# Kernel tuning notes

Hardware: AMD Instinct MI355X
Metric: run time of the kernel (lower is better)

## Reference

```python
import jax, jax.numpy as jnp
import numpy as np

N, G = 10000, 200          # nodes, graphs
EL, EG = 160000, 500000    # local / global edges
S, V = 256, 64             # scalar / vector hidden dims
NA, NB = 16, 5             # atom types, bond types


def _lin(k, i, o):
    return (jax.random.normal(k, (i, o), jnp.float32) / np.sqrt(i))


def scatter_mean(vals, idx, num_segments):
    # vals: [N, ...]; idx: [N] int
    sums = jax.ops.segment_sum(vals, idx, num_segments=num_segments)
    cnt = jax.ops.segment_sum(jnp.ones((vals.shape[0],), vals.dtype), idx,
                              num_segments=num_segments)
    cnt = jnp.maximum(cnt, 1.0).reshape((-1,) + (1,) * (vals.ndim - 1))
    return sums / cnt


def calc_edge_attrs(edge_index, pos):
    src, tgt = edge_index[0], edge_index[1]
    r = pos[tgt] - pos[src]                      # [E,3]
    a = (pos[tgt] * pos[src]).sum(-1)            # [E]
    d = jnp.sqrt(jnp.clip((r ** 2).sum(-1), 1e-6))
    r_norm = r / d[:, None]
    return d, a, r_norm


def setup_inputs() -> dict:
    key = jax.random.key(0)
    ks = jax.random.split(key, 24)
    inp = {}
    inp["x"] = jax.random.normal(ks[0], (N, NA), jnp.float32)
    inp["t"] = jax.random.uniform(ks[1], (G, 1), jnp.float32)
    inp["pos"] = jax.random.normal(ks[2], (N, 3), jnp.float32)
    eil = jax.random.randint(ks[3], (2, EL), 0, N)
    eig = jax.random.randint(ks[4], (2, EG), 0, N)
    # avoid self-edges so edge distances are strictly positive (safe sqrt grads)
    eig = eig.at[1].set(jnp.where(eig[1] == eig[0], (eig[1] + 1) % N, eig[1]))
    eil = eil.at[1].set(jnp.where(eil[1] == eil[0], (eil[1] + 1) % N, eil[1]))
    inp["edge_index_local"] = eil
    inp["edge_index_global"] = eig
    inp["edge_attr_global"] = jax.random.normal(ks[5], (EG, NB), jnp.float32)
    inp["batch"] = jnp.sort(jax.random.randint(ks[6], (N,), 0, G))
    # learned parameters
    inp["W_time"], inp["b_time"] = _lin(ks[7], 1, S), jnp.zeros((S,), jnp.float32)
    inp["W_atom"], inp["b_atom"] = _lin(ks[8], NA, S), jnp.zeros((S,), jnp.float32)
    inp["W_at"], inp["b_at"] = _lin(ks[9], S, S), jnp.zeros((S,), jnp.float32)
    inp["W_shared"], inp["b_shared"] = _lin(ks[10], S, S), jnp.zeros((S,), jnp.float32)
    inp["W_b0"], inp["b_b0"] = _lin(ks[11], S + 1, S), jnp.zeros((S,), jnp.float32)
    inp["W_b1"], inp["b_b1"] = _lin(ks[12], S, 2 * NB), jnp.zeros((2 * NB,), jnp.float32)
    inp["W_coord"] = _lin(ks[13], V, 2)           # no bias
    inp["W_atoms"], inp["b_atoms"] = _lin(ks[14], S, 2 * NA), jnp.zeros((2 * NA,), jnp.float32)
    return inp


def reference(x, t, pos, edge_attr_global, W_time, b_time, W_atom, b_atom,
              W_at, b_at, W_shared, b_shared, W_b0, b_b0, W_b1, b_b1,
              W_coord, W_atoms, b_atoms,
              edge_index_local, edge_index_global, batch):
    # --- trunk: center positions, embed atoms + time ---
    pos = pos - scatter_mean(pos, batch, G)[batch]
    temb = t @ W_time + b_time                    # [G,S]
    tnode = temb[batch]                           # [N,S]
    s = x @ W_atom + b_atom
    s = (s + tnode) @ W_at + b_at                 # [N,S]
    # --- edge attrs (gather-compute pattern feeding the GNN) ---
    d_l, a_l, rn_l = calc_edge_attrs(edge_index_local, pos)
    d_g, a_g, rn_g = calc_edge_attrs(edge_index_global, pos)
    # GNN stand-in (identity on s, v, p): v initialized to zeros as in original
    v = jnp.zeros((N, 3, V), s.dtype)
    # --- prediction head ---
    s = jax.nn.silu(s @ W_shared + b_shared)
    j, i = edge_index_global[0], edge_index_global[1]
    d = jnp.sqrt(((pos[i] - pos[j]) ** 2).sum(-1, keepdims=True))  # [EG,1]
    edge = jnp.concatenate([s[i] + s[j], d], axis=-1)              # [EG,S+1]
    bonds = jax.nn.silu(edge @ W_b0 + b_b0) @ W_b1 + b_b1          # [EG,2*NB]
    bonds_pred, bonds_eps = bonds[:, :NB], bonds[:, NB:]
    coords = jnp.einsum('nkv,vo->nko', v, W_coord)                 # [N,3,2]
    coords = coords - scatter_mean(coords, batch, G)[batch]
    coords_eps0, coords_eps1 = coords[..., 0], coords[..., 1]      # [N,3]
    atoms = s @ W_atoms + b_atoms                                  # [N,2*NA]
    atoms_eps, atoms_pred = atoms[:, :NA], atoms[:, NA:]
    pos_c = pos - scatter_mean(pos, batch, G)[batch]
    coords_pred = pos_c + coords_eps1
    return (coords_pred, coords_eps0, atoms_pred, atoms_eps,
            bonds_pred, bonds_eps, d_l, rn_l, a_g, rn_g)
```

## Files before the change

kernel.cpp:

```cpp
#include <hip/hip_runtime.h>
#include <hip/hip_bf16.h>

typedef __hip_bfloat16 bf16;
typedef short bf16x8 __attribute__((ext_vector_type(8)));
typedef float f32x4 __attribute__((ext_vector_type(4)));
typedef float f32x2 __attribute__((ext_vector_type(2)));

#define N_NODES  10000
#define G_GRAPHS 200
#define EL_EDGES 160000
#define EG_EDGES 500000
#define S_DIM    256
#define APAD     264

#define BONDS_BLOCKS 15625
#define LOCAL_BLOCKS 625
#define B1ROW    280

#define WS_FLAG   0
#define WS_POSC   1024
#define WS_WD     31232
#define WS_BB1    34304
#define WS_WATOM  34560
#define WS_WTIME  38656
#define WS_BTIME  38912
#define WS_BATOM  39168
#define WS_BAT    39424
#define WS_BSH    39680
#define WS_BATOMS 39936
#define WS_T      40000
#define WS_X      40448
#define WT_AT     200448
#define WT_SH     233216
#define WT_B0     265984
#define WT_ATOMS  298752
#define WS_B1F8   302848
#define WS_H      303968
#define WS_BB0R   943968
#define WS_END_FLOATS 944224

#define CHAN(S)    ((((S) >> 6) << 6) + (((S) & 3) << 4) + (((S) & 63) >> 2))
#define CHANINV(k) ((((k) >> 6) << 6) + (((k) & 15) << 2) + (((k) >> 4) & 3))

#define O_CPRED 0
#define O_CEPS  30000
#define O_APRED 60000
#define O_AEPS  220000
#define O_BPRED 380000
#define O_BEPS  2880000
#define O_DL    5380000
#define O_RNL   5540000
#define O_AG    6020000
#define O_RNG   6520000

__device__ __forceinline__ float b2f(bf16 v) { return __bfloat162float(v); }
__device__ __forceinline__ bf16  f2b(float v) { return __float2bfloat16(v); }
__device__ __forceinline__ unsigned short bbits(float v) {
    bf16 b = f2b(v);
    return *reinterpret_cast<unsigned short*>(&b);
}
__device__ __forceinline__ float ldin(const void* p, int idx, int isf32) {
    return isf32 ? ((const float*)p)[idx] : b2f(((const bf16*)p)[idx]);
}
__device__ __forceinline__ void stout(void* out, int f32o, size_t idx, float v) {
    if (f32o) ((float*)out)[idx] = v;
    else      ((bf16*)out)[idx]  = f2b(v);
}
__device__ __forceinline__ float silu(float p) {
    return p * __builtin_amdgcn_rcpf(1.0f + __expf(-p));
}
__device__ __forceinline__ int dtype_f32(const void* tt) {
    const unsigned short* q = (const unsigned short*)tt;
    int c = 0;
#pragma unroll
    for (int z = 0; z < 32; ++z) c += (q[z] >= 0x4000) ? 1 : 0;
    return c > 0;
}

__global__ void k_prep(const void* __restrict__ x, const void* __restrict__ tt,
                       const void* __restrict__ W_time, const void* __restrict__ b_time,
                       const void* __restrict__ W_atom, const void* __restrict__ b_atom,
                       const void* __restrict__ W_at, const void* __restrict__ b_at,
                       const void* __restrict__ W_shared, const void* __restrict__ b_shared,
                       const void* __restrict__ W_b0, const void* __restrict__ b_b0,
                       const void* __restrict__ W_b1, const void* __restrict__ b_b1,
                       const void* __restrict__ W_atoms, const void* __restrict__ b_atoms,
                       float* __restrict__ ws) {
    const int t = blockIdx.x * blockDim.x + threadIdx.x;
    const int f = dtype_f32(tt);
    if (t == 0) ws[WS_FLAG] = f ? 1.0f : 0.0f;
    if (t < 65536) {
        const int k = t >> 8, n = t & 255;
        ((unsigned short*)(ws + WT_AT))[n * 256 + k] = bbits(ldin(W_at, t, f));
        ((unsigned short*)(ws + WT_SH))[n * 256 + k] = bbits(ldin(W_shared, t, f));
        ((unsigned short*)(ws + WT_B0))[n * 256 + k] = bbits(ldin(W_b0, t, f));
    }
    if (t < 160000) ws[WS_X + t] = ldin(x, t, f);
    if (t < 8192) {
        const int k = t >> 5, n = t & 31;
        ((unsigned short*)(ws + WT_ATOMS))[n * 256 + k] = bbits(ldin(W_atoms, t, f));
    }
    if (t < 4480) {
        const int n = t / B1ROW, s = t - n * B1ROW;
        float v = (n < 10 && s < 256) ? ldin(W_b1, CHAN(s) * 10 + n, f) : 0.0f;
        int enc = __builtin_amdgcn_cvt_pk_fp8_f32(v, 0.0f, 0, false);
        ((unsigned char*)(ws + WS_B1F8))[t] = (unsigned char)(enc & 0xff);
    }
    if (t < 4096) ws[WS_WATOM + t] = ldin(W_atom, t, f);
    if (t < 256) {
        ws[WS_WD + t]   = ldin(W_b0, 65536 + CHAN(t), f);
        ws[WS_BB0R + t] = ldin(b_b0, t, f);
        ws[WS_WTIME + t] = ldin(W_time, t, f);
        ws[WS_BTIME + t] = ldin(b_time, t, f);
        ws[WS_BATOM + t] = ldin(b_atom, t, f);
        ws[WS_BAT + t]   = ldin(b_at, t, f);
        ws[WS_BSH + t]   = ldin(b_shared, t, f);
    }
    if (t < 200) ws[WS_T + t] = ldin(tt, t, f);
    if (t < 32)  ws[WS_BATOMS + t] = ldin(b_atoms, t, f);
    if (t < 16)  ws[WS_BB1 + t] = (t < 10) ? ldin(b_b1, t, f) : 0.0f;
}

__global__ void k_pos(const void* __restrict__ pos, const int* __restrict__ batch,
                      float* __restrict__ ws, void* __restrict__ out) {
    const int g = blockIdx.x;
    const int f32o = ws[WS_FLAG] != 0.0f;
    __shared__ int s_lo, s_hi;
    __shared__ float wsum[4][3];
    __shared__ float mean[3];
    if (threadIdx.x == 0) {
        int lo = 0, hi = N_NODES;
        while (lo < hi) { int m = (lo + hi) >> 1; if (batch[m] < g) lo = m + 1; else hi = m; }
        s_lo = lo;
        int lo2 = lo; hi = N_NODES;
        while (lo2 < hi) { int m = (lo2 + hi) >> 1; if (batch[m] < g + 1) lo2 = m + 1; else hi = m; }
        s_hi = lo2;
    }
    __syncthreads();
    const int lo = s_lo, hi = s_hi, cnt = hi - lo;
    float sx = 0.f, sy = 0.f, sz = 0.f;
    for (int n = lo + threadIdx.x; n < hi; n += 256) {
        sx += ldin(pos, n * 3 + 0, f32o);
        sy += ldin(pos, n * 3 + 1, f32o);
        sz += ldin(pos, n * 3 + 2, f32o);
    }
#pragma unroll
    for (int off = 32; off > 0; off >>= 1) {
        sx += __shfl_down(sx, off);
        sy += __shfl_down(sy, off);
        sz += __shfl_down(sz, off);
    }
    if ((threadIdx.x & 63) == 0) {
        wsum[threadIdx.x >> 6][0] = sx;
        wsum[threadIdx.x >> 6][1] = sy;
        wsum[threadIdx.x >> 6][2] = sz;
    }
    __syncthreads();
    if (threadIdx.x == 0) {
        float inv = 1.0f / (float)max(cnt, 1);
        mean[0] = (wsum[0][0] + wsum[1][0] + wsum[2][0] + wsum[3][0]) * inv;
        mean[1] = (wsum[0][1] + wsum[1][1] + wsum[2][1] + wsum[3][1]) * inv;
        mean[2] = (wsum[0][2] + wsum[1][2] + wsum[2][2] + wsum[3][2]) * inv;
    }
    __syncthreads();
    for (int n = lo + threadIdx.x; n < hi; n += 256) {
#pragma unroll
        for (int k = 0; k < 3; ++k) {
            float p = ldin(pos, n * 3 + k, f32o) - mean[k];
            ws[WS_POSC + n * 3 + k] = p;
            stout(out, f32o, O_CPRED + n * 3 + k, p);
            stout(out, f32o, O_CEPS + n * 3 + k, 0.0f);
        }
    }
}

__global__ __launch_bounds__(256) void k_node(
    const int* __restrict__ batch, const float* __restrict__ ws,
    unsigned int* __restrict__ h_out, void* __restrict__ out) {
    __shared__ unsigned short actA[16][APAD];
    __shared__ unsigned short actB[16][APAD];
    const int tid = threadIdx.x;
    const int wave = tid >> 6, lane = tid & 63;
    const int quad = lane >> 4, l16 = lane & 15;
    const int row0 = blockIdx.x * 16;

    {
        const int r = tid >> 4;
        const int c0 = (tid & 15) * 16;
        const int g = row0 + r;
        float tb = ws[WS_T + batch[g]];
        float xr[16];
#pragma unroll
        for (int k = 0; k < 16; ++k) xr[k] = ws[WS_X + g * 16 + k];
        for (int cc = 0; cc < 16; cc += 4) {
            const int c = c0 + cc;
            float a0 = ws[WS_BATOM + c + 0] + tb * ws[WS_WTIME + c + 0] + ws[WS_BTIME + c + 0];
            float a1 = ws[WS_BATOM + c + 1] + tb * ws[WS_WTIME + c + 1] + ws[WS_BTIME + c + 1];
            float a2 = ws[WS_BATOM + c + 2] + tb * ws[WS_WTIME + c + 2] + ws[WS_BTIME + c + 2];
            float a3 = ws[WS_BATOM + c + 3] + tb * ws[WS_WTIME + c + 3] + ws[WS_BTIME + c + 3];
#pragma unroll
            for (int k = 0; k < 16; ++k) {
                float4 w4 = *(const float4*)(ws + WS_WATOM + k * S_DIM + c);
                a0 += xr[k] * w4.x; a1 += xr[k] * w4.y;
                a2 += xr[k] * w4.z; a3 += xr[k] * w4.w;
            }
            actA[r][c + 0] = bbits(a0); actA[r][c + 1] = bbits(a1);
            actA[r][c + 2] = bbits(a2); actA[r][c + 3] = bbits(a3);
        }
    }
    __syncthreads();

    const unsigned short* wt_at = (const unsigned short*)(ws + WT_AT);
    const unsigned short* wt_sh = (const unsigned short*)(ws + WT_SH);
    const unsigned short* wt_b0 = (const unsigned short*)(ws + WT_B0);
    const unsigned short* wt_am = (const unsigned short*)(ws + WT_ATOMS);
    const int n0 = wave * 64;

    {
        f32x4 acc[4] = {};
        for (int kk = 0; kk < S_DIM; kk += 32) {
            const int k = kk + quad * 8;
            bf16x8 a = *(const bf16x8*)&actA[l16][k];
#pragma unroll
            for (int nt = 0; nt < 4; ++nt) {
                bf16x8 b = *(const bf16x8*)(wt_at + (size_t)(n0 + nt * 16 + l16) * S_DIM + k);
                acc[nt] = __builtin_amdgcn_mfma_f32_16x16x32_bf16(a, b, acc[nt], 0, 0, 0);
            }
        }
#pragma unroll
        for (int nt = 0; nt < 4; ++nt) {
            const int n = n0 + nt * 16 + l16;
            const float bv = ws[WS_BAT + n];
#pragma unroll
            for (int r = 0; r < 4; ++r)
                actB[quad * 4 + r][n] = bbits(acc[nt][r] + bv);
        }
    }
    __syncthreads();

    {
        f32x4 acc[4] = {};
        for (int kk = 0; kk < S_DIM; kk += 32) {
            const int k = kk + quad * 8;
            bf16x8 a = *(const bf16x8*)&actB[l16][k];
#pragma unroll
            for (int nt = 0; nt < 4; ++nt) {
                bf16x8 b = *(const bf16x8*)(wt_sh + (size_t)(n0 + nt * 16 + l16) * S_DIM + k);
                acc[nt] = __builtin_amdgcn_mfma_f32_16x16x32_bf16(a, b, acc[nt], 0, 0, 0);
            }
        }
        __syncthreads();
#pragma unroll
        for (int nt = 0; nt < 4; ++nt) {
            const int n = n0 + nt * 16 + l16;
            const float bv = ws[WS_BSH + n];
#pragma unroll
            for (int r = 0; r < 4; ++r)
                actA[quad * 4 + r][n] = bbits(silu(acc[nt][r] + bv));
        }
    }
    __syncthreads();

    {
        f32x4 acc[4] = {};
        for (int kk = 0; kk < S_DIM; kk += 32) {
            const int k = kk + quad * 8;
            bf16x8 a = *(const bf16x8*)&actA[l16][k];
#pragma unroll
            for (int nt = 0; nt < 4; ++nt) {
                bf16x8 b = *(const bf16x8*)(wt_b0 + (size_t)(n0 + nt * 16 + l16) * S_DIM + k);
                acc[nt] = __builtin_amdgcn_mfma_f32_16x16x32_bf16(a, b, acc[nt], 0, 0, 0);
            }
        }
        float bh[4];
#pragma unroll
        for (int nt = 0; nt < 4; ++nt) bh[nt] = 0.5f * ws[WS_BB0R + n0 + nt * 16 + l16];
#pragma unroll
        for (int r = 0; r < 4; ++r) {
            const int g = row0 + quad * 4 + r;
            int w = 0;
            w = __builtin_amdgcn_cvt_pk_fp8_f32(acc[0][r] + bh[0], acc[1][r] + bh[1], w, false);
            w = __builtin_amdgcn_cvt_pk_fp8_f32(acc[2][r] + bh[2], acc[3][r] + bh[3], w, true);
            h_out[(size_t)g * 64 + wave * 16 + l16] = (unsigned int)w;
        }
    }

    if (wave < 2) {
        f32x4 acc = {};
        const int n = wave * 16 + l16;
        for (int kk = 0; kk < S_DIM; kk += 32) {
            const int k = kk + quad * 8;
            bf16x8 a = *(const bf16x8*)&actA[l16][k];
            bf16x8 b = *(const bf16x8*)(wt_am + (size_t)n * S_DIM + k);
            acc = __builtin_amdgcn_mfma_f32_16x16x32_bf16(a, b, acc, 0, 0, 0);
        }
        const float bv = ws[WS_BATOMS + n];
        const int f32o = ws[WS_FLAG] != 0.0f;
#pragma unroll
        for (int r = 0; r < 4; ++r) {
            const int g = row0 + quad * 4 + r;
            float v = acc[r] + bv;
            if (n < 16) stout(out, f32o, O_AEPS + (size_t)g * 16 + n, v);
            else        stout(out, f32o, O_APRED + (size_t)g * 16 + (n - 16), v);
        }
    }
}

__global__ __launch_bounds__(256, 7) void k_edges(const int* __restrict__ eig,
                                                  const int* __restrict__ eil,
                                                  const float* __restrict__ ws,
                                                  const unsigned char* __restrict__ h,
                                                  void* __restrict__ out) {
    __shared__ unsigned char sm[2][32][272];
    __shared__ float cwd[256];
    __shared__ long cwb1l[16 * B1ROW / 8];
    unsigned char* cwb1 = (unsigned char*)cwb1l;
    const int f32o = ws[WS_FLAG] != 0.0f;

    if (blockIdx.x >= BONDS_BLOCKS) {
        const int e = (blockIdx.x - BONDS_BLOCKS) * 256 + threadIdx.x;
        const float* posc = ws + WS_POSC;
        const int s = eil[e];
        const int t = eil[EL_EDGES + e];
        float rx = posc[t * 3 + 0] - posc[s * 3 + 0];
        float ry = posc[t * 3 + 1] - posc[s * 3 + 1];
        float rz = posc[t * 3 + 2] - posc[s * 3 + 2];
        float dsq = rx * rx + ry * ry + rz * rz;
        float d = sqrtf(fmaxf(dsq, 1e-6f));
        float inv = 1.0f / d;
        stout(out, f32o, O_DL + e, d);
        stout(out, f32o, O_RNL + (size_t)e * 3 + 0, rx * inv);
        stout(out, f32o, O_RNL + (size_t)e * 3 + 1, ry * inv);
        stout(out, f32o, O_RNL + (size_t)e * 3 + 2, rz * inv);
        return;
    }

    {
        const int t = threadIdx.x;
        cwd[t] = ws[WS_WD + t];
        const unsigned int* src = (const unsigned int*)(ws + WS_B1F8);
        unsigned int* dst = (unsigned int*)cwb1;
        for (int q = t; q < 16 * B1ROW / 4; q += 256) dst[q] = src[q];
    }

    const int wave = threadIdx.x >> 6, lane = threadIdx.x & 63;
    const int quad = lane >> 4, l16 = lane & 15;
    const int P = wave >> 1, sub = wave & 1;
    const int e0 = blockIdx.x * 32 + P * 16;

    uint4 tmp[4];
#pragma unroll
    for (int p = 0; p < 4; ++p) {
        const int r16 = p * 4 + quad;
        const int es = e0 + r16;
        const int node = sub ? eig[es] : eig[EG_EDGES + es];
        tmp[p] = *(const uint4*)(h + (size_t)node * 256 + l16 * 16);
    }
#pragma unroll
    for (int p = 0; p < 4; ++p) {
        const int row = sub * 16 + p * 4 + quad;
        *(uint4*)&sm[P][row][l16 * 16] = tmp[p];
    }

    if (sub == 0) {
        const int e = e0 + l16;
        const int j = eig[e];
        const int i = eig[EG_EDGES + e];
        const float* posc = ws + WS_POSC;
        float pix = posc[i * 3 + 0], piy = posc[i * 3 + 1], piz = posc[i * 3 + 2];
        float pjx = posc[j * 3 + 0], pjy = posc[j * 3 + 1], pjz = posc[j * 3 + 2];
        float rx = pix - pjx, ry = piy - pjy, rz = piz - pjz;
        float dsq = rx * rx + ry * ry + rz * rz;
        if (quad == 0) {
            float ag = pix * pjx + piy * pjy + piz * pjz;
            float inv = 1.0f / sqrtf(fmaxf(dsq, 1e-6f));
            stout(out, f32o, O_AG + e, ag);
            stout(out, f32o, O_RNG + (size_t)e * 3 + 0, rx * inv);
            stout(out, f32o, O_RNG + (size_t)e * 3 + 1, ry * inv);
            stout(out, f32o, O_RNG + (size_t)e * 3 + 2, rz * inv);
            *(float*)&sm[P][l16][256] = sqrtf(dsq);
        }
    }
    __syncthreads();

    const float d = *(const float*)&sm[P][l16][256];
    const unsigned char* cw = cwb1 + (size_t)l16 * B1ROW;

    const int kbase = sub * 128;
    f32x4 acc = {};
#pragma unroll
    for (int t = 0; t < 4; ++t) {
        const int k = kbase + t * 32 + quad * 8;
        uint2 uaw = *(const uint2*)&sm[P][l16][k];
        uint2 ubw = *(const uint2*)&sm[P][16 + l16][k];
        float4 wA = *(const float4*)(cwd + k);
        float4 wB = *(const float4*)(cwd + k + 4);
        f32x2 a01 = __builtin_amdgcn_cvt_pk_f32_fp8((int)uaw.x, false);
        f32x2 a23 = __builtin_amdgcn_cvt_pk_f32_fp8((int)uaw.x, true);
        f32x2 a45 = __builtin_amdgcn_cvt_pk_f32_fp8((int)uaw.y, false);
        f32x2 a67 = __builtin_amdgcn_cvt_pk_f32_fp8((int)uaw.y, true);
        f32x2 b01 = __builtin_amdgcn_cvt_pk_f32_fp8((int)ubw.x, false);
        f32x2 b23 = __builtin_amdgcn_cvt_pk_f32_fp8((int)ubw.x, true);
        f32x2 b45 = __builtin_amdgcn_cvt_pk_f32_fp8((int)ubw.y, false);
        f32x2 b67 = __builtin_amdgcn_cvt_pk_f32_fp8((int)ubw.y, true);
        float u0 = silu(fmaf(d, wA.x, a01.x + b01.x));
        float u1 = silu(fmaf(d, wA.y, a01.y + b01.y));
        float u2 = silu(fmaf(d, wA.z, a23.x + b23.x));
        float u3 = silu(fmaf(d, wA.w, a23.y + b23.y));
        float u4 = silu(fmaf(d, wB.x, a45.x + b45.x));
        float u5 = silu(fmaf(d, wB.y, a45.y + b45.y));
        float u6 = silu(fmaf(d, wB.z, a67.x + b67.x));
        float u7 = silu(fmaf(d, wB.w, a67.y + b67.y));
        int lo = __builtin_amdgcn_cvt_pk_fp8_f32(u0, u1, 0, false);
        lo = __builtin_amdgcn_cvt_pk_fp8_f32(u2, u3, lo, true);
        int hi = __builtin_amdgcn_cvt_pk_fp8_f32(u4, u5, 0, false);
        hi = __builtin_amdgcn_cvt_pk_fp8_f32(u6, u7, hi, true);
        long a64 = (long)(((unsigned long)(unsigned int)hi << 32) | (unsigned int)lo);
        long b64 = *(const long*)(cw + k);
        acc = __builtin_amdgcn_mfma_f32_16x16x32_fp8_fp8(a64, b64, acc, 0, 0, 0);
    }

    __syncthreads();
    f32x4* sc = (f32x4*)&sm[P][0][0];
    if (sub == 1) sc[lane] = acc;
    __syncthreads();
    if (sub == 0 && l16 < 10) {
        f32x4 o = sc[lane];
        const float bv = ws[WS_BB1 + l16];
#pragma unroll
        for (int r = 0; r < 4; ++r) {
            const int er = e0 + quad * 4 + r;
            float v = acc[r] + o[r] + bv;
            if (l16 < 5) stout(out, f32o, O_BPRED + (size_t)er * 5 + l16, v);
            else         stout(out, f32o, O_BEPS + (size_t)er * 5 + (l16 - 5), v);
        }
    }
}

extern "C" void kernel_launch(void* const* d_in, const int* in_sizes, int n_in,
                              void* d_out, int out_size, void* d_ws, size_t ws_size,
                              hipStream_t stream) {
    const void* x        = d_in[0];
    const void* t        = d_in[1];
    const void* pos      = d_in[2];
    const int*  eil      = (const int*)d_in[3];
    const int*  eig      = (const int*)d_in[4];
    const int*  batch    = (const int*)d_in[6];
    const void* W_time   = d_in[7];
    const void* b_time   = d_in[8];
    const void* W_atom   = d_in[9];
    const void* b_atom   = d_in[10];
    const void* W_at     = d_in[11];
    const void* b_at     = d_in[12];
    const void* W_shared = d_in[13];
    const void* b_shared = d_in[14];
    const void* W_b0     = d_in[15];
    const void* b_b0     = d_in[16];
    const void* W_b1     = d_in[17];
    const void* b_b1     = d_in[18];
    const void* W_atoms  = d_in[20];
    const void* b_atoms  = d_in[21];
    (void)in_sizes; (void)n_in; (void)out_size;

    const size_t NEED = (size_t)WS_END_FLOATS * sizeof(float);
    if (ws_size < NEED) return;

    float* ws = (float*)d_ws;
    unsigned int* hbuf = (unsigned int*)(ws + WS_H);

    k_prep<<<640, 256, 0, stream>>>(x, t, W_time, b_time, W_atom, b_atom,
                                    W_at, b_at, W_shared, b_shared, W_b0, b_b0,
                                    W_b1, b_b1, W_atoms, b_atoms, ws);
    k_pos<<<G_GRAPHS, 256, 0, stream>>>(pos, batch, ws, d_out);
    k_node<<<N_NODES / 16, 256, 0, stream>>>(batch, ws, hbuf, d_out);
    k_edges<<<BONDS_BLOCKS + LOCAL_BLOCKS, 256, 0, stream>>>(
        eig, eil, ws, (const unsigned char*)hbuf, d_out);
}
```

Before: 224.4 us.

## Switch edge bond MLP to fp16 gathers with packed half silu and f16 MFMA

The per-node hidden projection is now stored as fp16 instead of fp8, and the edge kernel gathers both endpoint rows directly from global memory. One wave now handles 16 edges over the full K=256, so the LDS staging, the two-wave split-K and its reduction barriers are gone. The silu is computed in packed half precision with v_exp_f16/v_rcp_f16, and the second layer uses f16 MFMA with a pre-swizzled fp16 W_b1. This removes fp8 conversions and block syncs, but doubles gather bytes per edge and lowers the occupancy hint from 7 to 4.

```diff
diff --git a/kernel.cpp b/kernel.cpp
--- a/kernel.cpp
+++ b/kernel.cpp
@@ -4,7 +4,8 @@
 typedef __hip_bfloat16 bf16;
 typedef short bf16x8 __attribute__((ext_vector_type(8)));
 typedef float f32x4 __attribute__((ext_vector_type(4)));
-typedef float f32x2 __attribute__((ext_vector_type(2)));
+typedef _Float16 f16x2 __attribute__((ext_vector_type(2)));
+typedef _Float16 f16x8 __attribute__((ext_vector_type(8)));
 
 #define N_NODES  10000
 #define G_GRAPHS 200
@@ -13,13 +14,14 @@
 #define S_DIM    256
 #define APAD     264
 
-#define BONDS_BLOCKS 15625
-#define LOCAL_BLOCKS 625
-#define B1ROW    280
+#define BONDS2        7813
+#define LOCAL_BLOCKS  625
 
 #define WS_FLAG   0
 #define WS_POSC   1024
-#define WS_WD     31232
+#define WS_WDH    31232
+#define WS_W1F    31488
+#define WS_BB0R   33536
 #define WS_BB1    34304
 #define WS_WATOM  34560
 #define WS_WTIME  38656
@@ -34,13 +36,8 @@
 #define WT_SH     233216
 #define WT_B0     265984
 #define WT_ATOMS  298752
-#define WS_B1F8   302848
 #define WS_H      303968
-#define WS_BB0R   943968
-#define WS_END_FLOATS 944224
-
-#define CHAN(S)    ((((S) >> 6) << 6) + (((S) & 3) << 4) + (((S) & 63) >> 2))
-#define CHANINV(k) ((((k) >> 6) << 6) + (((k) & 15) << 2) + (((k) >> 4) & 3))
+#define WS_END_FLOATS 1583968
 
 #define O_CPRED 0
 #define O_CEPS  30000
@@ -59,6 +56,10 @@
     bf16 b = f2b(v);
     return *reinterpret_cast<unsigned short*>(&b);
 }
+__device__ __forceinline__ unsigned short h16bits(float v) {
+    _Float16 h = (_Float16)v;
+    return *reinterpret_cast<unsigned short*>(&h);
+}
 __device__ __forceinline__ float ldin(const void* p, int idx, int isf32) {
     return isf32 ? ((const float*)p)[idx] : b2f(((const bf16*)p)[idx]);
 }
@@ -68,6 +69,21 @@
 }
 __device__ __forceinline__ float silu(float p) {
     return p * __builtin_amdgcn_rcpf(1.0f + __expf(-p));
+}
+__device__ __forceinline__ _Float16 h_exp2(_Float16 x) {
+    _Float16 r;
+    asm("v_exp_f16 %0, %1" : "=v"(r) : "v"(x));
+    return r;
+}
+__device__ __forceinline__ _Float16 h_rcp(_Float16 x) {
+    _Float16 r;
+    asm("v_rcp_f16 %0, %1" : "=v"(r) : "v"(x));
+    return r;
+}
+__device__ __forceinline__ _Float16 h_silu(_Float16 p) {
+    const _Float16 nlog2e = (_Float16)(-1.44269504f);
+    _Float16 ex = h_exp2(p * nlog2e);
+    return p * h_rcp((_Float16)1.0f + ex);
 }
 __device__ __forceinline__ int dtype_f32(const void* tt) {
     const unsigned short* q = (const unsigned short*)tt;
@@ -100,15 +116,15 @@
         const int k = t >> 5, n = t & 31;
         ((unsigned short*)(ws + WT_ATOMS))[n * 256 + k] = bbits(ldin(W_atoms, t, f));
     }
-    if (t < 4480) {
-        const int n = t / B1ROW, s = t - n * B1ROW;
-        float v = (n < 10 && s < 256) ? ldin(W_b1, CHAN(s) * 10 + n, f) : 0.0f;
-        int enc = __builtin_amdgcn_cvt_pk_fp8_f32(v, 0.0f, 0, false);
-        ((unsigned char*)(ws + WS_B1F8))[t] = (unsigned char)(enc & 0xff);
+    if (t < 4096) {
+        const int i = t & 7, l16 = (t >> 3) & 15, quad = (t >> 7) & 3, ts = t >> 9;
+        const int k = ts * 32 + quad * 8 + i;
+        float v = (l16 < 10) ? ldin(W_b1, k * 10 + l16, f) : 0.0f;
+        ((unsigned short*)(ws + WS_W1F))[t] = h16bits(v);
     }
     if (t < 4096) ws[WS_WATOM + t] = ldin(W_atom, t, f);
     if (t < 256) {
-        ws[WS_WD + t]   = ldin(W_b0, 65536 + CHAN(t), f);
+        ((unsigned short*)(ws + WS_WDH))[t] = h16bits(ldin(W_b0, 65536 + t, f));
         ws[WS_BB0R + t] = ldin(b_b0, t, f);
         ws[WS_WTIME + t] = ldin(W_time, t, f);
         ws[WS_BTIME + t] = ldin(b_time, t, f);
@@ -176,7 +192,7 @@
 
 __global__ __launch_bounds__(256) void k_node(
     const int* __restrict__ batch, const float* __restrict__ ws,
-    unsigned int* __restrict__ h_out, void* __restrict__ out) {
+    unsigned short* __restrict__ h_out, void* __restrict__ out) {
     __shared__ unsigned short actA[16][APAD];
     __shared__ unsigned short actB[16][APAD];
     const int tid = threadIdx.x;
@@ -272,16 +288,16 @@
                 acc[nt] = __builtin_amdgcn_mfma_f32_16x16x32_bf16(a, b, acc[nt], 0, 0, 0);
             }
         }
-        float bh[4];
-#pragma unroll
-        for (int nt = 0; nt < 4; ++nt) bh[nt] = 0.5f * ws[WS_BB0R + n0 + nt * 16 + l16];
-#pragma unroll
-        for (int r = 0; r < 4; ++r) {
-            const int g = row0 + quad * 4 + r;
-            int w = 0;
-            w = __builtin_amdgcn_cvt_pk_fp8_f32(acc[0][r] + bh[0], acc[1][r] + bh[1], w, false);
-            w = __builtin_amdgcn_cvt_pk_fp8_f32(acc[2][r] + bh[2], acc[3][r] + bh[3], w, true);
-            h_out[(size_t)g * 64 + wave * 16 + l16] = (unsigned int)w;
+        _Float16* hp = (_Float16*)h_out;
+#pragma unroll
+        for (int nt = 0; nt < 4; ++nt) {
+            const int n = n0 + nt * 16 + l16;
+            const float bh = 0.5f * ws[WS_BB0R + n];
+#pragma unroll
+            for (int r = 0; r < 4; ++r) {
+                const int g = row0 + quad * 4 + r;
+                hp[(size_t)g * 256 + n] = (_Float16)(acc[nt][r] + bh);
+            }
         }
     }
 
@@ -306,19 +322,17 @@
     }
 }
 
-__global__ __launch_bounds__(256, 7) void k_edges(const int* __restrict__ eig,
+union H8 { f16x8 v; f16x2 p[4]; };
+
+__global__ __launch_bounds__(256, 4) void k_edges(const int* __restrict__ eig,
                                                   const int* __restrict__ eil,
                                                   const float* __restrict__ ws,
-                                                  const unsigned char* __restrict__ h,
+                                                  const _Float16* __restrict__ h,
                                                   void* __restrict__ out) {
-    __shared__ unsigned char sm[2][32][272];
-    __shared__ float cwd[256];
-    __shared__ long cwb1l[16 * B1ROW / 8];
-    unsigned char* cwb1 = (unsigned char*)cwb1l;
     const int f32o = ws[WS_FLAG] != 0.0f;
 
-    if (blockIdx.x >= BONDS_BLOCKS) {
-        const int e = (blockIdx.x - BONDS_BLOCKS) * 256 + threadIdx.x;
+    if (blockIdx.x >= BONDS2) {
+        const int e = (blockIdx.x - BONDS2) * 256 + threadIdx.x;
         const float* posc = ws + WS_POSC;
         const int s = eil[e];
         const int t = eil[EL_EDGES + e];
@@ -335,102 +349,63 @@
         return;
     }
 
-    {
-        const int t = threadIdx.x;
-        cwd[t] = ws[WS_WD + t];
-        const unsigned int* src = (const unsigned int*)(ws + WS_B1F8);
-        unsigned int* dst = (unsigned int*)cwb1;
-        for (int q = t; q < 16 * B1ROW / 4; q += 256) dst[q] = src[q];
-    }
-
     const int wave = threadIdx.x >> 6, lane = threadIdx.x & 63;
     const int quad = lane >> 4, l16 = lane & 15;
-    const int P = wave >> 1, sub = wave & 1;
-    const int e0 = blockIdx.x * 32 + P * 16;
-
-    uint4 tmp[4];
-#pragma unroll
-    for (int p = 0; p < 4; ++p) {
-        const int r16 = p * 4 + quad;
-        const int es = e0 + r16;
-        const int node = sub ? eig[es] : eig[EG_EDGES + es];
-        tmp[p] = *(const uint4*)(h + (size_t)node * 256 + l16 * 16);
-    }
-#pragma unroll
-    for (int p = 0; p < 4; ++p) {
-        const int row = sub * 16 + p * 4 + quad;
-        *(uint4*)&sm[P][row][l16 * 16] = tmp[p];
-    }
-
-    if (sub == 0) {
-        const int e = e0 + l16;
-        const int j = eig[e];
-        const int i = eig[EG_EDGES + e];
-        const float* posc = ws + WS_POSC;
-        float pix = posc[i * 3 + 0], piy = posc[i * 3 + 1], piz = posc[i * 3 + 2];
-        float pjx = posc[j * 3 + 0], pjy = posc[j * 3 + 1], pjz = posc[j * 3 + 2];
-        float rx = pix - pjx, ry = piy - pjy, rz = piz - pjz;
-        float dsq = rx * rx + ry * ry + rz * rz;
-        if (quad == 0) {
-            float ag = pix * pjx + piy * pjy + piz * pjz;
-            float inv = 1.0f / sqrtf(fmaxf(dsq, 1e-6f));
-            stout(out, f32o, O_AG + e, ag);
-            stout(out, f32o, O_RNG + (size_t)e * 3 + 0, rx * inv);
-            stout(out, f32o, O_RNG + (size_t)e * 3 + 1, ry * inv);
-            stout(out, f32o, O_RNG + (size_t)e * 3 + 2, rz * inv);
-            *(float*)&sm[P][l16][256] = sqrtf(dsq);
-        }
-    }
-    __syncthreads();
-
-    const float d = *(const float*)&sm[P][l16][256];
-    const unsigned char* cw = cwb1 + (size_t)l16 * B1ROW;
-
-    const int kbase = sub * 128;
+    const int e0 = blockIdx.x * 64 + wave * 16;
+    if (e0 >= EG_EDGES) return;
+
+    const int e = e0 + l16;
+    const int j = eig[e];
+    const int i = eig[EG_EDGES + e];
+
+    const float* posc = ws + WS_POSC;
+    float pix = posc[i * 3 + 0], piy = posc[i * 3 + 1], piz = posc[i * 3 + 2];
+    float pjx = posc[j * 3 + 0], pjy = posc[j * 3 + 1], pjz = posc[j * 3 + 2];
+    float rx = pix - pjx, ry = piy - pjy, rz = piz - pjz;
+    float dsq = rx * rx + ry * ry + rz * rz;
+    float dbf = sqrtf(dsq);
+    if (quad == 0) {
+        float ag = pix * pjx + piy * pjy + piz * pjz;
+        float inv = 1.0f / sqrtf(fmaxf(dsq, 1e-6f));
+        stout(out, f32o, O_AG + e, ag);
+        stout(out, f32o, O_RNG + (size_t)e * 3 + 0, rx * inv);
+        stout(out, f32o, O_RNG + (size_t)e * 3 + 1, ry * inv);
+        stout(out, f32o, O_RNG + (size_t)e * 3 + 2, rz * inv);
+    }
+
+    const _Float16 hd = (_Float16)dbf;
+    const f16x2 d2 = {hd, hd};
+
+    const _Float16* hi_row = h + (size_t)i * 256 + quad * 8;
+    const _Float16* hj_row = h + (size_t)j * 256 + quad * 8;
+    const _Float16* wdh = (const _Float16*)(ws + WS_WDH) + quad * 8;
+    const _Float16* w1f = (const _Float16*)(ws + WS_W1F) + (quad * 16 + l16) * 8;
+
     f32x4 acc = {};
-#pragma unroll
-    for (int t = 0; t < 4; ++t) {
-        const int k = kbase + t * 32 + quad * 8;
-        uint2 uaw = *(const uint2*)&sm[P][l16][k];
-        uint2 ubw = *(const uint2*)&sm[P][16 + l16][k];
-        float4 wA = *(const float4*)(cwd + k);
-        float4 wB = *(const float4*)(cwd + k + 4);
-        f32x2 a01 = __builtin_amdgcn_cvt_pk_f32_fp8((int)uaw.x, false);
-        f32x2 a23 = __builtin_amdgcn_cvt_pk_f32_fp8((int)uaw.x, true);
-        f32x2 a45 = __builtin_amdgcn_cvt_pk_f32_fp8((int)uaw.y, false);
-        f32x2 a67 = __builtin_amdgcn_cvt_pk_f32_fp8((int)uaw.y, true);
-        f32x2 b01 = __builtin_amdgcn_cvt_pk_f32_fp8((int)ubw.x, false);
-        f32x2 b23 = __builtin_amdgcn_cvt_pk_f32_fp8((int)ubw.x, true);
-        f32x2 b45 = __builtin_amdgcn_cvt_pk_f32_fp8((int)ubw.y, false);
-        f32x2 b67 = __builtin_amdgcn_cvt_pk_f32_fp8((int)ubw.y, true);
-        float u0 = silu(fmaf(d, wA.x, a01.x + b01.x));
-        float u1 = silu(fmaf(d, wA.y, a01.y + b01.y));
-        float u2 = silu(fmaf(d, wA.z, a23.x + b23.x));
-        float u3 = silu(fmaf(d, wA.w, a23.y + b23.y));
-        float u4 = silu(fmaf(d, wB.x, a45.x + b45.x));
-        float u5 = silu(fmaf(d, wB.y, a45.y + b45.y));
-        float u6 = silu(fmaf(d, wB.z, a67.x + b67.x));
-        float u7 = silu(fmaf(d, wB.w, a67.y + b67.y));
-        int lo = __builtin_amdgcn_cvt_pk_fp8_f32(u0, u1, 0, false);
-        lo = __builtin_amdgcn_cvt_pk_fp8_f32(u2, u3, lo, true);
-        int hi = __builtin_amdgcn_cvt_pk_fp8_f32(u4, u5, 0, false);
-        hi = __builtin_amdgcn_cvt_pk_fp8_f32(u6, u7, hi, true);
-        long a64 = (long)(((unsigned long)(unsigned int)hi << 32) | (unsigned int)lo);
-        long b64 = *(const long*)(cw + k);
-        acc = __builtin_amdgcn_mfma_f32_16x16x32_fp8_fp8(a64, b64, acc, 0, 0, 0);
-    }
-
-    __syncthreads();
-    f32x4* sc = (f32x4*)&sm[P][0][0];
-    if (sub == 1) sc[lane] = acc;
-    __syncthreads();
-    if (sub == 0 && l16 < 10) {
-        f32x4 o = sc[lane];
+#pragma unroll 2
+    for (int t = 0; t < 8; ++t) {
+        H8 A, B, W;
+        A.v = *(const f16x8*)(hi_row + t * 32);
+        B.v = *(const f16x8*)(hj_row + t * 32);
+        W.v = *(const f16x8*)(wdh + t * 32);
+        f16x8 WB = *(const f16x8*)(w1f + t * 512);
+        f16x2 p2[4];
+#pragma unroll
+        for (int pp = 0; pp < 4; ++pp)
+            p2[pp] = (A.p[pp] + B.p[pp]) + d2 * W.p[pp];
+        f16x8 U = {h_silu(p2[0][0]), h_silu(p2[0][1]),
+                   h_silu(p2[1][0]), h_silu(p2[1][1]),
+                   h_silu(p2[2][0]), h_silu(p2[2][1]),
+                   h_silu(p2[3][0]), h_silu(p2[3][1])};
+        acc = __builtin_amdgcn_mfma_f32_16x16x32_f16(U, WB, acc, 0, 0, 0);
+    }
+
+    if (l16 < 10) {
         const float bv = ws[WS_BB1 + l16];
 #pragma unroll
         for (int r = 0; r < 4; ++r) {
             const int er = e0 + quad * 4 + r;
-            float v = acc[r] + o[r] + bv;
+            float v = acc[r] + bv;
             if (l16 < 5) stout(out, f32o, O_BPRED + (size_t)er * 5 + l16, v);
             else         stout(out, f32o, O_BEPS + (size_t)er * 5 + (l16 - 5), v);
         }
@@ -466,13 +441,13 @@
     if (ws_size < NEED) return;
 
     float* ws = (float*)d_ws;
-    unsigned int* hbuf = (unsigned int*)(ws + WS_H);
+    unsigned short* hbuf = (unsigned short*)(ws + WS_H);
 
     k_prep<<<640, 256, 0, stream>>>(x, t, W_time, b_time, W_atom, b_atom,
                                     W_at, b_at, W_shared, b_shared, W_b0, b_b0,
                                     W_b1, b_b1, W_atoms, b_atoms, ws);
     k_pos<<<G_GRAPHS, 256, 0, stream>>>(pos, batch, ws, d_out);
     k_node<<<N_NODES / 16, 256, 0, stream>>>(batch, ws, hbuf, d_out);
-    k_edges<<<BONDS_BLOCKS + LOCAL_BLOCKS, 256, 0, stream>>>(
-        eig, eil, ws, (const unsigned char*)hbuf, d_out);
-}
+    k_edges<<<BONDS2 + LOCAL_BLOCKS, 256, 0, stream>>>(
+        eig, eil, ws, (const _Float16*)hbuf, d_out);
+}
```

Measured after the change: 252.6 us. 12.6% more time.
